# Kernel optimization log

Hardware: AMD Instinct MI355X
Metric: run time of the kernel (lower is better)

Reference implementation:

```python
import jax, jax.numpy as jnp
import numpy as np

DIM = 192
NUM_HEADS = 6
WINDOW = (2, 6, 12)
INPUT_RES = (8, 48, 180)
TYPE_OF_WINDOWS = (INPUT_RES[0] // WINDOW[0]) * (INPUT_RES[1] // WINDOW[1])  # 32
N_TOK = WINDOW[0] * WINDOW[1] * WINDOW[2]  # 144
NLON = INPUT_RES[2] // WINDOW[2]  # 15
TABLE_ROWS = WINDOW[0] ** 2 * WINDOW[1] ** 2 * (2 * WINDOW[2] - 1)  # 3312


def calculate_position_bias_indices(ws):
    wz, wh, ww = ws
    zi = np.arange(wz)
    zj = -np.arange(wz) * wz
    hi = np.arange(wh)
    hj = -np.arange(wh) * wh
    w = np.arange(ww)
    c1 = np.stack(np.meshgrid(zi, hi, w, indexing='ij')).reshape(3, -1)
    c2 = np.stack(np.meshgrid(zj, hj, w, indexing='ij')).reshape(3, -1)
    coords = (c1[:, :, None] - c2[:, None, :]).transpose(1, 2, 0).copy()
    coords[:, :, 2] += ww - 1
    coords[:, :, 1] *= 2 * ww - 1
    coords[:, :, 0] *= (2 * ww - 1) * wh * wh
    return coords.sum(-1)  # (N, N) in [0, TABLE_ROWS)


def setup_inputs() -> dict:
    key = jax.random.key(0)
    ks = jax.random.split(key, 7)
    B_ = NLON  # batch=1 times nLon window columns
    x = jax.random.normal(ks[0], (B_, TYPE_OF_WINDOWS, N_TOK, DIM), dtype=jnp.float32)
    mask = jax.random.normal(ks[1], (NLON, TYPE_OF_WINDOWS, N_TOK, N_TOK), dtype=jnp.float32)
    qkv_w = jax.random.normal(ks[2], (3 * DIM, DIM), dtype=jnp.float32) * 0.02
    qkv_b = jax.random.normal(ks[3], (3 * DIM,), dtype=jnp.float32) * 0.02
    proj_w = jax.random.normal(ks[4], (DIM, DIM), dtype=jnp.float32) * 0.02
    proj_b = jax.random.normal(ks[5], (DIM,), dtype=jnp.float32) * 0.02
    bias_table = jax.random.normal(ks[6], (TABLE_ROWS, TYPE_OF_WINDOWS, NUM_HEADS), dtype=jnp.float32) * 0.02
    position_index = jnp.asarray(calculate_position_bias_indices(WINDOW), dtype=jnp.int64)
    return {"x": x, "mask": mask, "qkv_w": qkv_w, "qkv_b": qkv_b,
            "proj_w": proj_w, "proj_b": proj_b, "bias_table": bias_table,
            "position_index": position_index}


def reference(x, mask, qkv_w, qkv_b, proj_w, proj_b, bias_table, position_index):
    B_, nW_, N, C = x.shape
    H = NUM_HEADS
    hd = C // H
    scale = hd ** (-0.5)
    # qkv projection: (B_, nW_, N, 3, H, hd)
    qkv = (jnp.einsum('bwnc,dc->bwnd', x, qkv_w) + qkv_b).reshape(B_, nW_, N, 3, H, hd)
    q = qkv[:, :, :, 0] * scale  # (B_, nW_, N, H, hd)
    k = qkv[:, :, :, 1]
    v = qkv[:, :, :, 2]
    # attention scores: (B_, H, nW_, N, N)
    attn = jnp.einsum('bwihd,bwjhd->bhwij', q, k)
    # gathered earth position bias -> (H, nW_, N, N)
    bias = bias_table[position_index.reshape(-1)]  # (N*N, nW_, H)
    bias = bias.reshape(N, N, nW_, H).transpose(3, 2, 0, 1)
    attn = attn + bias[None]
    # mask add: view (B_//nLon, nLon, H, nW_, N, N) + mask (nLon, 1, nW_, N, N)
    nLon = mask.shape[0]
    attn = attn.reshape(B_ // nLon, nLon, H, nW_, N, N) + mask[None, :, None]
    attn = attn.reshape(B_, H, nW_, N, N)
    attn = jax.nn.softmax(attn, axis=-1)
    out = jnp.einsum('bhwij,bwjhd->bwihd', attn, v).reshape(B_, nW_, N, C)
    out = jnp.einsum('bwnc,dc->bwnd', out, proj_w) + proj_b
    return out
```

## Files before the change

### kernel.cpp

```cpp
#include <hip/hip_runtime.h>
#include <hip/hip_bf16.h>

#define B_LON 15
#define NW    32
#define NTOK  144
#define DIM   192
#define NH    6
#define HD    32
#define K3    576
#define MROWS (B_LON*NW*NTOK)
#define NN    (NTOK*NTOK)
#define SCALE 0.17677669529663687f

typedef __attribute__((ext_vector_type(8))) short bf16x8;
typedef __attribute__((ext_vector_type(8))) unsigned short u16x8;
typedef __attribute__((ext_vector_type(4))) float f32x4;

__device__ inline unsigned short f2bf(float f) {
  __bf16 h = (__bf16)f;
  return __builtin_bit_cast(unsigned short, h);
}
__device__ inline float bf2f(unsigned short u) {
  union { unsigned int i; float f; } c;
  c.i = ((unsigned int)u) << 16;
  return c.f;
}

#define NX8 1658880
#define NQ8 13824
#define NP8 4608

__global__ __launch_bounds__(256) void conv_bf_k(
    const float* __restrict__ x, const float* __restrict__ qw,
    const float* __restrict__ pw,
    unsigned short* __restrict__ xbf, unsigned short* __restrict__ qwbf,
    unsigned short* __restrict__ pwbf) {
  const long gid = (long)blockIdx.x * 256 + threadIdx.x;
  const float* src;
  unsigned short* dst;
  long off;
  if (gid < NX8)            { src = x;  dst = xbf;  off = gid; }
  else if (gid < NX8 + NQ8) { src = qw; dst = qwbf; off = gid - NX8; }
  else                      { src = pw; dst = pwbf; off = gid - NX8 - NQ8; }
  const float4 a = ((const float4*)src)[off * 2];
  const float4 b = ((const float4*)src)[off * 2 + 1];
  u16x8 u = {f2bf(a.x), f2bf(a.y), f2bf(a.z), f2bf(a.w),
             f2bf(b.x), f2bf(b.y), f2bf(b.z), f2bf(b.w)};
  *(u16x8*)&dst[off * 8] = u;
}

__global__ __launch_bounds__(256) void bias_pre_k(
    const float* __restrict__ btab, const int* __restrict__ pos,
    unsigned short* __restrict__ biasb) {
  const int wh  = blockIdx.x;
  const int seg = blockIdx.y * 2304;
  unsigned short* dst = biasb + (size_t)wh * NN;
#pragma unroll
  for (int it = 0; it < 9; ++it) {
    const int e = seg + it * 256 + threadIdx.x;
    dst[e] = f2bf(btab[(size_t)pos[e] * (NW * NH) + wh]);
  }
}

__global__ __launch_bounds__(256) void qkv_gemm_k(
    const unsigned short* __restrict__ X, const unsigned short* __restrict__ W,
    const float* __restrict__ Bv,
    unsigned short* __restrict__ qb, unsigned short* __restrict__ kb,
    unsigned short* __restrict__ vb) {
  __shared__ unsigned short As[64 * 200];
  __shared__ unsigned short Bs[64 * 200];
  const int t    = threadIdx.x;
  const int n0   = blockIdx.x * 64;
  const int m0   = blockIdx.y * 64;
  const int w    = t >> 6;
  const int lane = t & 63;
  const int ln15 = lane & 15;
  const int quad = lane >> 4;

#pragma unroll
  for (int it = t; it < 1536; it += 256) {
    const int row = it / 24;
    const int c8  = (it % 24) * 8;
    *(u16x8*)&As[row * 200 + c8] = *(const u16x8*)&X[(size_t)(m0 + row) * 192 + c8];
  }
#pragma unroll
  for (int it = t; it < 1536; it += 256) {
    const int row = it / 24;
    const int c8  = (it % 24) * 8;
    *(u16x8*)&Bs[row * 200 + c8] = *(const u16x8*)&W[(size_t)(n0 + row) * 192 + c8];
  }
  __syncthreads();

  f32x4 acc[4];
#pragma unroll
  for (int j = 0; j < 4; ++j) acc[j] = (f32x4){0.f, 0.f, 0.f, 0.f};

#pragma unroll
  for (int k0 = 0; k0 < 192; k0 += 32) {
    const bf16x8 af = *(bf16x8*)&As[(w * 16 + ln15) * 200 + k0 + quad * 8];
#pragma unroll
    for (int nt = 0; nt < 4; ++nt) {
      const bf16x8 bfr = *(bf16x8*)&Bs[(nt * 16 + ln15) * 200 + k0 + quad * 8];
      acc[nt] = __builtin_amdgcn_mfma_f32_16x16x32_bf16(af, bfr, acc[nt], 0, 0, 0);
    }
  }

  const int s   = n0 / 192;
  const int nr  = n0 % 192;
  const float sc2 = (s == 0) ? SCALE : 1.0f;
  unsigned short* dst = (s == 0) ? qb : (s == 1 ? kb : vb);
#pragma unroll
  for (int nt = 0; nt < 4; ++nt) {
    const int colg = n0 + nt * 16 + ln15;
    const int h    = (nr + nt * 16 + ln15) >> 5;
    const int dd   = (nr + nt * 16 + ln15) & 31;
    const float bias = Bv[colg];
#pragma unroll
    for (int r = 0; r < 4; ++r) {
      const int m  = m0 + w * 16 + quad * 4 + r;
      const int bw = m / NTOK;
      const int n  = m % NTOK;
      const unsigned short val = f2bf((acc[nt][r] + bias) * sc2);
      if (s < 2)
        dst[((size_t)(bw * NH + h) * NTOK + n) * HD + dd] = val;
      else
        dst[((size_t)(bw * NH + h) * HD + dd) * NTOK + n] = val;
    }
  }
}

__global__ __launch_bounds__(192, 3) void attn_k(
    const unsigned short* __restrict__ qbuf, const unsigned short* __restrict__ kbuf,
    const unsigned short* __restrict__ vbuf, const float* __restrict__ mask,
    const unsigned short* __restrict__ biasb, unsigned short* __restrict__ ao) {
  __shared__ unsigned short Ks[NTOK * 36];
  __shared__ unsigned short Vs[32 * 160];
  __shared__ unsigned short Ps[3 * 16 * 168];

  const int t    = threadIdx.x;
  const int wave = t / 64;
  const int lane = t & 63;
  const int ln15 = lane & 15;
  const int quad = lane >> 4;
  const int idx  = blockIdx.x;
  const int h    = idx / 480;
  const int bw   = idx % 480;
  const int w    = bw & 31;
  const int wh   = w * NH + h;
  const size_t hb = (size_t)(bw * NH + h) * (NTOK * HD);
  const unsigned short* qh = qbuf + hb;
  const float* maskp = mask + (size_t)bw * NN;
  const unsigned short* biasp = biasb + (size_t)wh * NN;
  unsigned short* ps = &Ps[wave * 16 * 168];

  for (int it = t; it < 576; it += 192) {
    const int row = it >> 2;
    const int col = (it & 3) * 8;
    *(u16x8*)&Ks[row * 36 + col] = *(const u16x8*)&kbuf[hb + row * HD + col];
  }
  for (int it = t; it < 576; it += 192) {
    const int row = it / 18;
    const int col = (it % 18) * 8;
    *(u16x8*)&Vs[row * 160 + col] = *(const u16x8*)&vbuf[hb + row * NTOK + col];
  }
  if (t < 64) {
    u16x8 z = {0, 0, 0, 0, 0, 0, 0, 0};
    *(u16x8*)&Vs[(t >> 1) * 160 + 144 + (t & 1) * 8] = z;
  }
  {
    ushort4 z = {0, 0, 0, 0};
    *(ushort4*)&ps[(lane >> 2) * 168 + 144 + (lane & 3) * 4] = z;
  }
  __syncthreads();

  for (int g = wave * 3; g < wave * 3 + 3; ++g) {
    const int i0 = g * 16;
    const int ib = i0 + quad * 4;

    const bf16x8 qf = *(const bf16x8*)&qh[(i0 + ln15) * HD + quad * 8];
    f32x4 s[9];
#pragma unroll
    for (int jt = 0; jt < 9; ++jt) {
      const bf16x8 kf = *(const bf16x8*)&Ks[(jt * 16 + ln15) * 36 + quad * 8];
      s[jt] = (f32x4){0.f, 0.f, 0.f, 0.f};
      s[jt] = __builtin_amdgcn_mfma_f32_16x16x32_bf16(qf, kf, s[jt], 0, 0, 0);
    }

#pragma unroll
    for (int jt = 0; jt < 9; ++jt) {
      const int j = jt * 16 + ln15;
#pragma unroll
      for (int r = 0; r < 4; ++r) {
        const int ij = (ib + r) * NTOK + j;
        s[jt][r] += bf2f(biasp[ij]) + maskp[ij];
      }
    }

    float rinv[4];
#pragma unroll
    for (int r = 0; r < 4; ++r) {
      float mx = s[0][r];
#pragma unroll
      for (int jt = 1; jt < 9; ++jt) mx = fmaxf(mx, s[jt][r]);
#pragma unroll
      for (int off = 1; off < 16; off <<= 1) mx = fmaxf(mx, __shfl_xor(mx, off));
      float sum = 0.f;
#pragma unroll
      for (int jt = 0; jt < 9; ++jt) {
        const float e = __expf(s[jt][r] - mx);
        s[jt][r] = e;
        sum += e;
      }
#pragma unroll
      for (int off = 1; off < 16; off <<= 1) sum += __shfl_xor(sum, off);
      rinv[r] = 1.0f / sum;
    }

#pragma unroll
    for (int jt = 0; jt < 9; ++jt)
#pragma unroll
      for (int r = 0; r < 4; ++r)
        ps[(quad * 4 + r) * 168 + jt * 16 + ln15] = f2bf(s[jt][r]);

    f32x4 o[2] = {{0.f, 0.f, 0.f, 0.f}, {0.f, 0.f, 0.f, 0.f}};
#pragma unroll
    for (int kt = 0; kt < 5; ++kt) {
      const bf16x8 pf = *(const bf16x8*)&ps[ln15 * 168 + kt * 32 + quad * 8];
#pragma unroll
      for (int nt = 0; nt < 2; ++nt) {
        const bf16x8 vf = *(const bf16x8*)&Vs[(nt * 16 + ln15) * 160 + kt * 32 + quad * 8];
        o[nt] = __builtin_amdgcn_mfma_f32_16x16x32_bf16(pf, vf, o[nt], 0, 0, 0);
      }
    }

#pragma unroll
    for (int nt = 0; nt < 2; ++nt)
#pragma unroll
      for (int r = 0; r < 4; ++r)
        ao[(size_t)(bw * NTOK + ib + r) * DIM + h * HD + nt * 16 + ln15] =
            f2bf(o[nt][r] * rinv[r]);
  }
}

__global__ __launch_bounds__(256) void proj_gemm_k(
    const unsigned short* __restrict__ AO, const unsigned short* __restrict__ W,
    const float* __restrict__ Bv, float* __restrict__ out) {
  __shared__ unsigned short As[64 * 200];
  __shared__ unsigned short Bs[64 * 200];
  const int t    = threadIdx.x;
  const int n0   = blockIdx.x * 64;
  const int m0   = blockIdx.y * 64;
  const int w    = t >> 6;
  const int lane = t & 63;
  const int ln15 = lane & 15;
  const int quad = lane >> 4;

#pragma unroll
  for (int it = t; it < 1536; it += 256) {
    const int row = it / 24;
    const int c8  = (it % 24) * 8;
    *(u16x8*)&As[row * 200 + c8] = *(const u16x8*)&AO[(size_t)(m0 + row) * 192 + c8];
  }
#pragma unroll
  for (int it = t; it < 1536; it += 256) {
    const int row = it / 24;
    const int c8  = (it % 24) * 8;
    *(u16x8*)&Bs[row * 200 + c8] = *(const u16x8*)&W[(size_t)(n0 + row) * 192 + c8];
  }
  __syncthreads();

  f32x4 acc[4];
#pragma unroll
  for (int j = 0; j < 4; ++j) acc[j] = (f32x4){0.f, 0.f, 0.f, 0.f};

#pragma unroll
  for (int k0 = 0; k0 < 192; k0 += 32) {
    const bf16x8 af = *(bf16x8*)&As[(w * 16 + ln15) * 200 + k0 + quad * 8];
#pragma unroll
    for (int nt = 0; nt < 4; ++nt) {
      const bf16x8 bfr = *(bf16x8*)&Bs[(nt * 16 + ln15) * 200 + k0 + quad * 8];
      acc[nt] = __builtin_amdgcn_mfma_f32_16x16x32_bf16(af, bfr, acc[nt], 0, 0, 0);
    }
  }

#pragma unroll
  for (int nt = 0; nt < 4; ++nt) {
    const int colg = n0 + nt * 16 + ln15;
    const float bias = Bv[colg];
#pragma unroll
    for (int r = 0; r < 4; ++r) {
      const int m = m0 + w * 16 + quad * 4 + r;
      out[(size_t)m * 192 + colg] = acc[nt][r] + bias;
    }
  }
}

extern "C" void kernel_launch(void* const* d_in, const int* in_sizes, int n_in,
                              void* d_out, int out_size, void* d_ws, size_t ws_size,
                              hipStream_t stream) {
  const float* x      = (const float*)d_in[0];
  const float* mask   = (const float*)d_in[1];
  const float* qkv_w  = (const float*)d_in[2];
  const float* qkv_b  = (const float*)d_in[3];
  const float* proj_w = (const float*)d_in[4];
  const float* proj_b = (const float*)d_in[5];
  const float* btab   = (const float*)d_in[6];
  const int*   pos    = (const int*)d_in[7];
  float* out = (float*)d_out;

  unsigned short* ws = (unsigned short*)d_ws;
  const size_t sz = (size_t)MROWS * DIM;
  unsigned short* qbuf  = ws;
  unsigned short* kbuf  = ws + sz;
  unsigned short* vbuf  = ws + 2 * sz;
  unsigned short* aobuf = ws + 3 * sz + 256;
  unsigned short* biasb = ws + 4 * sz + 1024;
  unsigned short* xbf   = biasb + (size_t)192 * NN;
  unsigned short* qwbf  = xbf + sz;
  unsigned short* pwbf  = qwbf + (size_t)K3 * DIM;

  conv_bf_k<<<NX8 / 256 + NQ8 / 256 + NP8 / 256, 256, 0, stream>>>(
      x, qkv_w, proj_w, xbf, qwbf, pwbf);
  bias_pre_k<<<dim3(NW * NH, 9), 256, 0, stream>>>(btab, pos, biasb);
  qkv_gemm_k<<<dim3(K3 / 64, MROWS / 64), 256, 0, stream>>>(
      xbf, qwbf, qkv_b, qbuf, kbuf, vbuf);
  attn_k<<<NH * 480, 192, 0, stream>>>(
      qbuf, kbuf, vbuf, mask, biasb, aobuf);
  proj_gemm_k<<<dim3(DIM / 64, MROWS / 64), 256, 0, stream>>>(
      aobuf, pwbf, proj_b, out);
}
```

Before: 318.1 us.

## Fuse QKV projection into attention kernel per window-head block

Removes the separate QKV GEMM kernel. Each attention block now computes its own head's Q, K and V slices directly from bf16 X and the weights using MFMA, writing them into shared memory instead of global buffers. This avoids writing Q/K/V to global memory and reading them back, and saves one launch. In exchange, each block reloads X rows and weight rows straight from global memory with no shared-memory staging, and uses more registers (18 accumulators) and a new Qs shared array, which may limit occupancy.

```diff
diff --git a/kernel.cpp b/kernel.cpp
--- a/kernel.cpp
+++ b/kernel.cpp
@@ -62,77 +62,11 @@
   }
 }
 
-__global__ __launch_bounds__(256) void qkv_gemm_k(
+__global__ __launch_bounds__(192, 3) void fused_attn_k(
     const unsigned short* __restrict__ X, const unsigned short* __restrict__ W,
-    const float* __restrict__ Bv,
-    unsigned short* __restrict__ qb, unsigned short* __restrict__ kb,
-    unsigned short* __restrict__ vb) {
-  __shared__ unsigned short As[64 * 200];
-  __shared__ unsigned short Bs[64 * 200];
-  const int t    = threadIdx.x;
-  const int n0   = blockIdx.x * 64;
-  const int m0   = blockIdx.y * 64;
-  const int w    = t >> 6;
-  const int lane = t & 63;
-  const int ln15 = lane & 15;
-  const int quad = lane >> 4;
-
-#pragma unroll
-  for (int it = t; it < 1536; it += 256) {
-    const int row = it / 24;
-    const int c8  = (it % 24) * 8;
-    *(u16x8*)&As[row * 200 + c8] = *(const u16x8*)&X[(size_t)(m0 + row) * 192 + c8];
-  }
-#pragma unroll
-  for (int it = t; it < 1536; it += 256) {
-    const int row = it / 24;
-    const int c8  = (it % 24) * 8;
-    *(u16x8*)&Bs[row * 200 + c8] = *(const u16x8*)&W[(size_t)(n0 + row) * 192 + c8];
-  }
-  __syncthreads();
-
-  f32x4 acc[4];
-#pragma unroll
-  for (int j = 0; j < 4; ++j) acc[j] = (f32x4){0.f, 0.f, 0.f, 0.f};
-
-#pragma unroll
-  for (int k0 = 0; k0 < 192; k0 += 32) {
-    const bf16x8 af = *(bf16x8*)&As[(w * 16 + ln15) * 200 + k0 + quad * 8];
-#pragma unroll
-    for (int nt = 0; nt < 4; ++nt) {
-      const bf16x8 bfr = *(bf16x8*)&Bs[(nt * 16 + ln15) * 200 + k0 + quad * 8];
-      acc[nt] = __builtin_amdgcn_mfma_f32_16x16x32_bf16(af, bfr, acc[nt], 0, 0, 0);
-    }
-  }
-
-  const int s   = n0 / 192;
-  const int nr  = n0 % 192;
-  const float sc2 = (s == 0) ? SCALE : 1.0f;
-  unsigned short* dst = (s == 0) ? qb : (s == 1 ? kb : vb);
-#pragma unroll
-  for (int nt = 0; nt < 4; ++nt) {
-    const int colg = n0 + nt * 16 + ln15;
-    const int h    = (nr + nt * 16 + ln15) >> 5;
-    const int dd   = (nr + nt * 16 + ln15) & 31;
-    const float bias = Bv[colg];
-#pragma unroll
-    for (int r = 0; r < 4; ++r) {
-      const int m  = m0 + w * 16 + quad * 4 + r;
-      const int bw = m / NTOK;
-      const int n  = m % NTOK;
-      const unsigned short val = f2bf((acc[nt][r] + bias) * sc2);
-      if (s < 2)
-        dst[((size_t)(bw * NH + h) * NTOK + n) * HD + dd] = val;
-      else
-        dst[((size_t)(bw * NH + h) * HD + dd) * NTOK + n] = val;
-    }
-  }
-}
-
-__global__ __launch_bounds__(192, 3) void attn_k(
-    const unsigned short* __restrict__ qbuf, const unsigned short* __restrict__ kbuf,
-    const unsigned short* __restrict__ vbuf, const float* __restrict__ mask,
+    const float* __restrict__ Bv, const float* __restrict__ mask,
     const unsigned short* __restrict__ biasb, unsigned short* __restrict__ ao) {
+  __shared__ unsigned short Qs[NTOK * 36];
   __shared__ unsigned short Ks[NTOK * 36];
   __shared__ unsigned short Vs[32 * 160];
   __shared__ unsigned short Ps[3 * 16 * 168];
@@ -147,22 +81,11 @@
   const int bw   = idx % 480;
   const int w    = bw & 31;
   const int wh   = w * NH + h;
-  const size_t hb = (size_t)(bw * NH + h) * (NTOK * HD);
-  const unsigned short* qh = qbuf + hb;
   const float* maskp = mask + (size_t)bw * NN;
   const unsigned short* biasp = biasb + (size_t)wh * NN;
   unsigned short* ps = &Ps[wave * 16 * 168];
-
-  for (int it = t; it < 576; it += 192) {
-    const int row = it >> 2;
-    const int col = (it & 3) * 8;
-    *(u16x8*)&Ks[row * 36 + col] = *(const u16x8*)&kbuf[hb + row * HD + col];
-  }
-  for (int it = t; it < 576; it += 192) {
-    const int row = it / 18;
-    const int col = (it % 18) * 8;
-    *(u16x8*)&Vs[row * 160 + col] = *(const u16x8*)&vbuf[hb + row * NTOK + col];
-  }
+  const int wv3 = wave * 3;
+
   if (t < 64) {
     u16x8 z = {0, 0, 0, 0, 0, 0, 0, 0};
     *(u16x8*)&Vs[(t >> 1) * 160 + 144 + (t & 1) * 8] = z;
@@ -171,13 +94,56 @@
     ushort4 z = {0, 0, 0, 0};
     *(ushort4*)&ps[(lane >> 2) * 168 + 144 + (lane & 3) * 4] = z;
   }
+
+  f32x4 acc[3][6];
+#pragma unroll
+  for (int mt = 0; mt < 3; ++mt)
+#pragma unroll
+    for (int nt = 0; nt < 6; ++nt) acc[mt][nt] = (f32x4){0.f, 0.f, 0.f, 0.f};
+
+#pragma unroll
+  for (int kk = 0; kk < 6; ++kk) {
+    const int k0 = kk * 32 + quad * 8;
+    bf16x8 af[3], bfr[6];
+#pragma unroll
+    for (int mt = 0; mt < 3; ++mt)
+      af[mt] = *(const bf16x8*)&X[(size_t)(bw * NTOK + (wv3 + mt) * 16 + ln15) * DIM + k0];
+#pragma unroll
+    for (int nt = 0; nt < 6; ++nt) {
+      const int wrow = (nt >> 1) * DIM + h * HD + (nt & 1) * 16 + ln15;
+      bfr[nt] = *(const bf16x8*)&W[(size_t)wrow * DIM + k0];
+    }
+#pragma unroll
+    for (int mt = 0; mt < 3; ++mt)
+#pragma unroll
+      for (int nt = 0; nt < 6; ++nt)
+        acc[mt][nt] = __builtin_amdgcn_mfma_f32_16x16x32_bf16(
+            af[mt], bfr[nt], acc[mt][nt], 0, 0, 0);
+  }
+
+#pragma unroll
+  for (int nt = 0; nt < 6; ++nt) {
+    const int dd   = (nt & 1) * 16 + ln15;
+    const float bias = Bv[(nt >> 1) * DIM + h * HD + dd];
+#pragma unroll
+    for (int mt = 0; mt < 3; ++mt) {
+      const int tok = (wv3 + mt) * 16 + quad * 4;
+#pragma unroll
+      for (int r = 0; r < 4; ++r) {
+        const float v = acc[mt][nt][r] + bias;
+        if (nt < 2)      Qs[(tok + r) * 36 + dd] = f2bf(v * SCALE);
+        else if (nt < 4) Ks[(tok + r) * 36 + dd] = f2bf(v);
+        else             Vs[dd * 160 + tok + r]  = f2bf(v);
+      }
+    }
+  }
   __syncthreads();
 
-  for (int g = wave * 3; g < wave * 3 + 3; ++g) {
+  for (int g = wv3; g < wv3 + 3; ++g) {
     const int i0 = g * 16;
     const int ib = i0 + quad * 4;
 
-    const bf16x8 qf = *(const bf16x8*)&qh[(i0 + ln15) * HD + quad * 8];
+    const bf16x8 qf = *(const bf16x8*)&Qs[(i0 + ln15) * 36 + quad * 8];
     f32x4 s[9];
 #pragma unroll
     for (int jt = 0; jt < 9; ++jt) {
@@ -310,22 +276,17 @@
 
   unsigned short* ws = (unsigned short*)d_ws;
   const size_t sz = (size_t)MROWS * DIM;
-  unsigned short* qbuf  = ws;
-  unsigned short* kbuf  = ws + sz;
-  unsigned short* vbuf  = ws + 2 * sz;
-  unsigned short* aobuf = ws + 3 * sz + 256;
-  unsigned short* biasb = ws + 4 * sz + 1024;
-  unsigned short* xbf   = biasb + (size_t)192 * NN;
+  unsigned short* aobuf = ws;
+  unsigned short* biasb = ws + sz + 256;
+  unsigned short* xbf   = biasb + (size_t)192 * NN + 256;
   unsigned short* qwbf  = xbf + sz;
   unsigned short* pwbf  = qwbf + (size_t)K3 * DIM;
 
   conv_bf_k<<<NX8 / 256 + NQ8 / 256 + NP8 / 256, 256, 0, stream>>>(
       x, qkv_w, proj_w, xbf, qwbf, pwbf);
   bias_pre_k<<<dim3(NW * NH, 9), 256, 0, stream>>>(btab, pos, biasb);
-  qkv_gemm_k<<<dim3(K3 / 64, MROWS / 64), 256, 0, stream>>>(
-      xbf, qwbf, qkv_b, qbuf, kbuf, vbuf);
-  attn_k<<<NH * 480, 192, 0, stream>>>(
-      qbuf, kbuf, vbuf, mask, biasb, aobuf);
+  fused_attn_k<<<NH * 480, 192, 0, stream>>>(
+      xbf, qwbf, qkv_b, mask, biasb, aobuf);
   proj_gemm_k<<<dim3(DIM / 64, MROWS / 64), 256, 0, stream>>>(
       aobuf, pwbf, proj_b, out);
 }
```

New measurement: 290.8 us. 1.09x faster.
